# Optimization experiments

Measured on AMD Instinct MI355X. Metric: run time of the kernel, lower is better.

The kernel has to match this reference:

```python
import jax, jax.numpy as jnp
import numpy as np
from jax import lax

NUM_HEADS = 4
FIN = 4096
FOUT = 4096


def setup_inputs() -> dict:
    key = jax.random.key(0)
    k1, k2, k3, k4, k5 = jax.random.split(key, 5)
    inp = jax.random.normal(k1, (2, 2048, FIN), dtype=jnp.float32)
    # xavier-uniform-like scale for the fc weight
    lim = float(np.sqrt(6.0 / (FIN + FOUT)))
    W = jax.random.uniform(k2, (FOUT, FIN), minval=-lim, maxval=lim, dtype=jnp.float32)
    # per-head 3x3 conv kernels (Conv2d(1, 1, 3, 3) per head, stacked OIHW)
    conv_w = jax.random.normal(k3, (NUM_HEADS, 1, 3, 3), dtype=jnp.float32) * (1.0 / 3.0)
    conv_b = jax.random.normal(k4, (NUM_HEADS,), dtype=jnp.float32) * 0.1
    sk_wt = jax.random.normal(k5, (NUM_HEADS, 1, 1), dtype=jnp.float32)
    return {"inp": inp, "W": W, "conv_w": conv_w, "conv_b": conv_b, "sk_wt": sk_wt}


def _transform_weight(W, conv_w, conv_b, sk_wt):
    # W: [fout, fin] -> [num_heads, fout/num_heads, fin]
    mat = W.reshape(NUM_HEADS, FOUT // NUM_HEADS, FIN)
    # per-head 3x3 conv == grouped conv with feature_group_count = num_heads
    x = mat[None]  # [1, H=num_heads, fout/h, fin]
    y = lax.conv_general_dilated(
        x, conv_w,
        window_strides=(1, 1),
        padding=((1, 1), (1, 1)),
        feature_group_count=NUM_HEADS,
        dimension_numbers=("NCHW", "OIHW", "NCHW"),
    )[0] + conv_b[:, None, None]
    # sigmoid-gated residual: out + sigmoid(sk_wt) * mat
    out = y + jax.nn.sigmoid(sk_wt) * mat
    return out.reshape(FOUT, FIN)


def reference(inp, W, conv_w, conv_b, sk_wt):
    W_i = _transform_weight(W, conv_w, conv_b, sk_wt)
    # F.linear(inp, W_i) with bias=None
    return jnp.einsum("bsf,of->bso", inp, W_i)
```

## Files before the change

kernel.cpp:

```cpp
#include <hip/hip_runtime.h>
#include <hip/hip_bf16.h>

#define FIN 4096
#define FOUT 4096
#define HEADS 4
#define ROWS_PER_HEAD (FOUT / HEADS)
#define M_DIM 4096

typedef __attribute__((ext_vector_type(8))) short bf16x8;
typedef __attribute__((ext_vector_type(4))) float floatx4;

#define CAST_BLOCKS ((M_DIM * FIN) / (256 * 8))
#define TRANS_BLOCKS 2048

__global__ __launch_bounds__(256) void prep(
    const float* __restrict__ x,
    __hip_bfloat16* __restrict__ y,
    const float* __restrict__ W,
    const float* __restrict__ cw,
    const float* __restrict__ cb,
    const float* __restrict__ sk,
    __hip_bfloat16* __restrict__ Wt) {
  if (blockIdx.x < CAST_BLOCKS) {
    int idx = blockIdx.x * 256 + threadIdx.x;
    const float4* xv = (const float4*)x;
    float4 a = xv[idx * 2];
    float4 b = xv[idx * 2 + 1];
    __hip_bfloat16 t[8];
    t[0] = __float2bfloat16(a.x); t[1] = __float2bfloat16(a.y);
    t[2] = __float2bfloat16(a.z); t[3] = __float2bfloat16(a.w);
    t[4] = __float2bfloat16(b.x); t[5] = __float2bfloat16(b.y);
    t[6] = __float2bfloat16(b.z); t[7] = __float2bfloat16(b.w);
    *(bf16x8*)(&y[(size_t)idx * 8]) = *(bf16x8*)t;
    return;
  }

  int tg = blockIdx.x - CAST_BLOCKS;
  tg = (tg & 7) * (TRANS_BLOCKS / 8) + (tg >> 3);
  const int o0 = (tg >> 1) * 4;
  const int fs = (tg & 1) * 2048 + threadIdx.x * 8;
  const int h = o0 >> 10;
  const int r0 = o0 & (ROWS_PER_HEAD - 1);

  float kk[3][3];
#pragma unroll
  for (int i = 0; i < 3; i++)
#pragma unroll
    for (int j = 0; j < 3; j++) kk[i][j] = cw[h * 9 + i * 3 + j];
  float sig = 1.0f / (1.0f + __expf(-sk[h]));
  float bias = cb[h];

  float w[6][10];
#pragma unroll
  for (int i = 0; i < 6; i++) {
    int rr = r0 - 1 + i;
    if (rr < 0 || rr >= ROWS_PER_HEAD) {
#pragma unroll
      for (int c = 0; c < 10; c++) w[i][c] = 0.0f;
    } else {
      const float* rp = W + ((size_t)(h * ROWS_PER_HEAD + rr)) * FIN + fs;
      float4 v0 = *(const float4*)rp;
      float4 v1 = *(const float4*)(rp + 4);
      w[i][1] = v0.x; w[i][2] = v0.y; w[i][3] = v0.z; w[i][4] = v0.w;
      w[i][5] = v1.x; w[i][6] = v1.y; w[i][7] = v1.z; w[i][8] = v1.w;
      w[i][0] = (fs > 0) ? rp[-1] : 0.0f;
      w[i][9] = (fs + 8 < FIN) ? rp[8] : 0.0f;
    }
  }

#pragma unroll
  for (int j = 0; j < 4; j++) {
    float acc[8];
#pragma unroll
    for (int c = 0; c < 8; c++) acc[c] = bias + sig * w[j + 1][c + 1];
#pragma unroll
    for (int dr = 0; dr < 3; dr++) {
#pragma unroll
      for (int c = 0; c < 8; c++)
        acc[c] += kk[dr][0] * w[j + dr][c] + kk[dr][1] * w[j + dr][c + 1] +
                  kk[dr][2] * w[j + dr][c + 2];
    }
    __hip_bfloat16 t[8];
#pragma unroll
    for (int c = 0; c < 8; c++) t[c] = __float2bfloat16(acc[c]);
    *(bf16x8*)(&Wt[(size_t)(o0 + j) * FIN + fs]) = *(bf16x8*)t;
  }
}

__device__ static inline void gload_lds16(const void* g, void* l) {
  __builtin_amdgcn_global_load_lds(
      (const __attribute__((address_space(1))) void*)g,
      (__attribute__((address_space(3))) void*)l, 16, 0, 0);
}

#define BK 64
#define NT (FIN / BK)

__global__ __launch_bounds__(512, 2) void gemm_nt(
    const __hip_bfloat16* __restrict__ A,
    const __hip_bfloat16* __restrict__ B,
    float* __restrict__ C,
    int M, int N, int K) {
  __shared__ __hip_bfloat16 As0h0[128 * BK];
  __shared__ __hip_bfloat16 As0h1[128 * BK];
  __shared__ __hip_bfloat16 As1h0[128 * BK];
  __shared__ __hip_bfloat16 As1h1[128 * BK];
  __shared__ __hip_bfloat16 Bs0h0[128 * BK];
  __shared__ __hip_bfloat16 Bs0h1[128 * BK];
  __shared__ __hip_bfloat16 Bs1h0[128 * BK];
  __shared__ __hip_bfloat16 Bs1h1[128 * BK];

  const int tid = threadIdx.x;
  const int lane = tid & 63;
  const int wave = tid >> 6;
  const int wr = wave >> 2;
  const int wn = wave & 3;
  const int fr = lane & 15;
  const int quad = lane >> 4;
  const int sel = fr & 7;

  const int orig = blockIdx.y * gridDim.x + blockIdx.x;
  const int swz = (orig & 7) * 32 + (orig >> 3);
  const int tile_m = (swz >> 4) * 256;
  const int tile_n = (swz & 15) * 256;

  const __hip_bfloat16* At = A + (size_t)tile_m * K;
  const __hip_bfloat16* Bt = B + (size_t)tile_n * K;

  int soff[2], doff[2];
#pragma unroll
  for (int c = 0; c < 2; c++) {
    int p = c * 512 + tid;
    int row = p >> 3;
    int g = (p & 7) ^ (row & 7);
    soff[c] = row * K + g * 8;
    doff[c] = p * 8;
  }
  int aro[4], bro[2], co[2];
#pragma unroll
  for (int u = 0; u < 4; u++) aro[u] = (wr * 16 + u * 32 + fr) * 64;
#pragma unroll
  for (int j = 0; j < 2; j++) bro[j] = (wn * 16 + j * 64 + fr) * 64;
#pragma unroll
  for (int kk = 0; kk < 2; kk++) co[kk] = ((kk * 4 + quad) ^ sel) * 8;

  floatx4 acc[8][4];
#pragma unroll
  for (int i = 0; i < 8; i++)
#pragma unroll
    for (int j = 0; j < 4; j++) acc[i][j] = (floatx4){0.f, 0.f, 0.f, 0.f};

  bf16x8 afr[2][4];
  bf16x8 bfr[2][2][2];

#define STAGE(GBASE, DST, TILE, HALF)                                    \
  do {                                                                   \
    const __hip_bfloat16* _s =                                           \
        GBASE + (size_t)(HALF) * 128 * K + (size_t)(TILE) * BK;          \
    _Pragma("unroll") for (int _c = 0; _c < 2; _c++) {                   \
      gload_lds16(_s + soff[_c], DST + doff[_c]);                        \
    }                                                                    \
  } while (0)

#define LOADA4(MS, SRC, KK)                                              \
  do {                                                                   \
    _Pragma("unroll") for (int _u = 0; _u < 4; _u++) {                   \
      afr[MS][_u] = *(const bf16x8*)&SRC[aro[_u] + co[KK]];              \
    }                                                                    \
  } while (0)

#define LOADB2(KS, NH, SRC, KK)                                          \
  do {                                                                   \
    _Pragma("unroll") for (int _j = 0; _j < 2; _j++) {                   \
      bfr[KS][NH][_j] = *(const bf16x8*)&SRC[bro[_j] + co[KK]];          \
    }                                                                    \
  } while (0)

#define MMA8(MS, KS, NH)                                                 \
  do {                                                                   \
    __builtin_amdgcn_s_setprio(1);                                       \
    _Pragma("unroll") for (int _u = 0; _u < 4; _u++) {                   \
      _Pragma("unroll") for (int _j = 0; _j < 2; _j++) {                 \
        acc[(MS) * 4 + _u][(NH) * 2 + _j] =                              \
            __builtin_amdgcn_mfma_f32_16x16x32_bf16(                     \
                afr[MS][_u], bfr[KS][NH][_j],                            \
                acc[(MS) * 4 + _u][(NH) * 2 + _j], 0, 0, 0);             \
      }                                                                  \
    }                                                                    \
    __builtin_amdgcn_s_setprio(0);                                       \
  } while (0)

#define BAR() __builtin_amdgcn_s_barrier()
#define WAITVM(N) asm volatile("s_waitcnt vmcnt(" #N ")" ::: "memory")
#define FENCE_LGKM(N)                                                    \
  do {                                                                   \
    __builtin_amdgcn_sched_barrier(0);                                   \
    asm volatile("s_waitcnt lgkmcnt(" #N ")" ::: "memory");              \
    __builtin_amdgcn_sched_barrier(0);                                   \
  } while (0)

#define TBODY(T, CA0, CA1, CB0, CB1, NA0, NA1, NB0, NB1, DO_C8, DO_STAGE) \
  do {                                                                    \
    LOADA4(0, CA0, 0);                                                    \
    LOADB2(0, 0, CB0, 0);                                                 \
    LOADB2(0, 1, CB1, 0);                                                 \
    if (DO_C8) MMA8(1, 1, 0);                         \
    FENCE_LGKM(0);                                                        \
    MMA8(0, 0, 0);                                                \
    LOADA4(1, CA1, 0);                                           \
    MMA8(0, 0, 1);                                                \
    LOADB2(1, 0, CB0, 1);                                        \
    LOADB2(1, 1, CB1, 1);                                                 \
    LOADA4(0, CA0, 1);          \
    if (DO_STAGE) {                                                       \
      STAGE(At, NA0, (T) + 1, 0);                                         \
      STAGE(At, NA1, (T) + 1, 1);                                         \
    }                                                                     \
    FENCE_LGKM(8);                                                        \
    MMA8(1, 0, 1);                                                \
    MMA8(1, 0, 0);                                                \
    LOADA4(1, CA1, 1);                                           \
    FENCE_LGKM(4);                                                        \
    MMA8(0, 1, 0);                                                \
    if (DO_STAGE) {                                                       \
      STAGE(Bt, NB0, (T) + 1, 0);                                         \
      STAGE(Bt, NB1, (T) + 1, 1);                                         \
    }                                                                     \
    MMA8(0, 1, 1);                                                \
    FENCE_LGKM(0);                                                        \
    MMA8(1, 1, 1);                                                \
    if (DO_STAGE) WAITVM(0);                                              \
    BAR();                                                                \
  } while (0)

  STAGE(At, As0h0, 0, 0);
  STAGE(At, As0h1, 0, 1);
  STAGE(Bt, Bs0h0, 0, 0);
  STAGE(Bt, Bs0h1, 0, 1);
  WAITVM(0);
  BAR();

  TBODY(0, As0h0, As0h1, Bs0h0, Bs0h1, As1h0, As1h1, Bs1h0, Bs1h1, 0, 1);

#pragma unroll 1
  for (int t = 1; t < NT - 1; t += 2) {
    TBODY(t, As1h0, As1h1, Bs1h0, Bs1h1, As0h0, As0h1, Bs0h0, Bs0h1, 1, 1);
    TBODY(t + 1, As0h0, As0h1, Bs0h0, Bs0h1, As1h0, As1h1, Bs1h0, Bs1h1, 1, 1);
  }

  TBODY(NT - 1, As1h0, As1h1, Bs1h0, Bs1h1, As0h0, As0h1, Bs0h0, Bs0h1, 1, 0);
  MMA8(1, 1, 0);

#undef TBODY
#undef FENCE_LGKM
#undef STAGE
#undef LOADA4
#undef LOADB2
#undef MMA8
#undef BAR
#undef WAITVM

#pragma unroll
  for (int i = 0; i < 8; i++) {
    int mb = tile_m + wr * 16 + i * 32 + quad * 4;
#pragma unroll
    for (int j = 0; j < 4; j++) {
      int n = tile_n + wn * 16 + j * 64 + fr;
#pragma unroll
      for (int r = 0; r < 4; r++) {
        C[(size_t)(mb + r) * N + n] = acc[i][j][r];
      }
    }
  }
}

extern "C" void kernel_launch(void* const* d_in, const int* in_sizes, int n_in,
                              void* d_out, int out_size, void* d_ws,
                              size_t ws_size, hipStream_t stream) {
  const float* inp = (const float*)d_in[0];
  const float* W = (const float*)d_in[1];
  const float* conv_w = (const float*)d_in[2];
  const float* conv_b = (const float*)d_in[3];
  const float* sk_wt = (const float*)d_in[4];
  float* out = (float*)d_out;

  __hip_bfloat16* Wt = (__hip_bfloat16*)d_ws;
  __hip_bfloat16* Ab =
      (__hip_bfloat16*)((char*)d_ws + (size_t)(32u << 20));

  prep<<<CAST_BLOCKS + TRANS_BLOCKS, 256, 0, stream>>>(inp, Ab, W, conv_w,
                                                       conv_b, sk_wt, Wt);
  dim3 grid(FOUT / 256, M_DIM / 256);
  gemm_nt<<<grid, 512, 0, stream>>>(Ab, Wt, out, M_DIM, FOUT, FIN);
}
```

Before: 283.3 us.

## Deepen GEMM global-to-LDS prefetch to two tiles ahead with partial vmcnt waits

Restructures the main GEMM loop so global loads for tile t+2 are issued mid-iteration into buffers already consumed, and the remaining A half for t+1 at the top. The full vmcnt(0) drain is replaced by a partial vmcnt(6) wait, which keeps more loads in flight and hides more global-memory latency. An extra barrier is added mid-iteration to guard buffer reuse, and the prologue and epilogue are reworked for the deeper pipeline. This risks race or ordering bugs and adds barrier overhead.

After: 288.6 us. No clear change (+1.8%).

```diff
diff --git a/kernel.cpp b/kernel.cpp
--- a/kernel.cpp
+++ b/kernel.cpp
@@ -191,7 +191,7 @@
   } while (0)
 
 #define BAR() __builtin_amdgcn_s_barrier()
-#define WAITVM(N) asm volatile("s_waitcnt vmcnt(" #N ")" ::: "memory")
+#define VMC(N) asm volatile("s_waitcnt vmcnt(" #N ")" ::: "memory")
 #define FENCE_LGKM(N)                                                    \
   do {                                                                   \
     __builtin_amdgcn_sched_barrier(0);                                   \
@@ -199,56 +199,61 @@
     __builtin_amdgcn_sched_barrier(0);                                   \
   } while (0)
 
-#define TBODY(T, CA0, CA1, CB0, CB1, NA0, NA1, NB0, NB1, DO_C8, DO_STAGE) \
-  do {                                                                    \
-    LOADA4(0, CA0, 0);                                                    \
-    LOADB2(0, 0, CB0, 0);                                                 \
-    LOADB2(0, 1, CB1, 0);                                                 \
-    if (DO_C8) MMA8(1, 1, 0);                         \
-    FENCE_LGKM(0);                                                        \
-    MMA8(0, 0, 0);                                                \
-    LOADA4(1, CA1, 0);                                           \
-    MMA8(0, 0, 1);                                                \
-    LOADB2(1, 0, CB0, 1);                                        \
-    LOADB2(1, 1, CB1, 1);                                                 \
-    LOADA4(0, CA0, 1);          \
-    if (DO_STAGE) {                                                       \
-      STAGE(At, NA0, (T) + 1, 0);                                         \
-      STAGE(At, NA1, (T) + 1, 1);                                         \
-    }                                                                     \
-    FENCE_LGKM(8);                                                        \
-    MMA8(1, 0, 1);                                                \
-    MMA8(1, 0, 0);                                                \
-    LOADA4(1, CA1, 1);                                           \
-    FENCE_LGKM(4);                                                        \
-    MMA8(0, 1, 0);                                                \
-    if (DO_STAGE) {                                                       \
-      STAGE(Bt, NB0, (T) + 1, 0);                                         \
-      STAGE(Bt, NB1, (T) + 1, 1);                                         \
-    }                                                                     \
-    MMA8(0, 1, 1);                                                \
-    FENCE_LGKM(0);                                                        \
-    MMA8(1, 1, 1);                                                \
-    if (DO_STAGE) WAITVM(0);                                              \
-    BAR();                                                                \
+#define TBODY(T, CA0, CA1, CB0, CB1, NA1, DO_C8, DO_TOP, DO_MID, EVM)    \
+  do {                                                                   \
+    if (DO_TOP) STAGE(At, NA1, (T) + 1, 1);                              \
+    LOADA4(0, CA0, 0);                                          \
+    LOADB2(0, 0, CB0, 0);                                                \
+    LOADB2(0, 1, CB1, 0);                                                \
+    if (DO_C8) MMA8(1, 1, 0);                        \
+    FENCE_LGKM(0);                                                       \
+    MMA8(0, 0, 0);                                               \
+    LOADA4(1, CA1, 0);                                          \
+    MMA8(0, 0, 1);                                               \
+    LOADB2(1, 0, CB0, 1);                                       \
+    LOADB2(1, 1, CB1, 1);                                                \
+    LOADA4(0, CA0, 1);                                          \
+    FENCE_LGKM(8);                                                       \
+    MMA8(1, 0, 1);                                               \
+    MMA8(1, 0, 0);                                               \
+    LOADA4(1, CA1, 1);                                          \
+    FENCE_LGKM(4);                                                       \
+    BAR();      \
+    if (DO_MID) {                                                        \
+      STAGE(At, CA0, (T) + 2, 0);                                        \
+      STAGE(Bt, CB0, (T) + 2, 0);                                        \
+      STAGE(Bt, CB1, (T) + 2, 1);                                        \
+    }                                                                    \
+    MMA8(0, 1, 0);                                               \
+    MMA8(0, 1, 1);                                               \
+    FENCE_LGKM(0);                                                       \
+    MMA8(1, 1, 1);                                               \
+    if ((EVM) == 2) VMC(6);                                              \
+    else if ((EVM) == 1) VMC(0);                                         \
+    BAR();                                                               \
   } while (0)
 
   STAGE(At, As0h0, 0, 0);
-  STAGE(At, As0h1, 0, 1);
   STAGE(Bt, Bs0h0, 0, 0);
   STAGE(Bt, Bs0h1, 0, 1);
-  WAITVM(0);
+  STAGE(At, As0h1, 0, 1);
+  STAGE(Bt, Bs1h0, 1, 0);
+  STAGE(Bt, Bs1h1, 1, 1);
+  STAGE(At, As1h0, 1, 0);
+  VMC(6);
   BAR();
 
-  TBODY(0, As0h0, As0h1, Bs0h0, Bs0h1, As1h0, As1h1, Bs1h0, Bs1h1, 0, 1);
+  TBODY(0, As0h0, As0h1, Bs0h0, Bs0h1, As1h1, 0, 1, 1, 2);
 
 #pragma unroll 1
-  for (int t = 1; t < NT - 1; t += 2) {
-    TBODY(t, As1h0, As1h1, Bs1h0, Bs1h1, As0h0, As0h1, Bs0h0, Bs0h1, 1, 1);
-    TBODY(t + 1, As0h0, As0h1, Bs0h0, Bs0h1, As1h0, As1h1, Bs1h0, Bs1h1, 1, 1);
-  }
-
-  TBODY(NT - 1, As1h0, As1h1, Bs1h0, Bs1h1, As0h0, As0h1, Bs0h0, Bs0h1, 1, 0);
+  for (int t = 1; t < NT - 3; t += 2) {
+    TBODY(t, As1h0, As1h1, Bs1h0, Bs1h1, As0h1, 1, 1, 1, 2);
+    TBODY(t + 1, As0h0, As0h1, Bs0h0, Bs0h1, As1h1, 1, 1, 1, 2);
+  }
+
+  TBODY(NT - 3, As1h0, As1h1, Bs1h0, Bs1h1, As0h1, 1, 1, 1, 2);
+  TBODY(NT - 2, As0h0, As0h1, Bs0h0, Bs0h1, As1h1, 1, 1, 0, 1);
+  TBODY(NT - 1, As1h0, As1h1, Bs1h0, Bs1h1, As0h1, 1, 0, 0, 0);
   MMA8(1, 1, 0);
 
 #undef TBODY
@@ -258,7 +263,7 @@
 #undef LOADB2
 #undef MMA8
 #undef BAR
-#undef WAITVM
+#undef VMC
 
 #pragma unroll
   for (int i = 0; i < 8; i++) {
```
